# Performance work log

Hardware: AMD Instinct MI355X
Metric: run time of the kernel (lower is better)

Reference implementation:

```python
import jax, jax.numpy as jnp
import numpy as np

N_NODES = 100000
N_EDGES = 1600000
N_GRAPHS = 1024
EMB = 32
HID = 64
N_CLASSES = 10
N_SHAPE = 16
N_COLOR = 8


def setup_inputs() -> dict:
    key = jax.random.key(0)
    ks = jax.random.split(key, 12)
    shape_id = jax.random.randint(ks[0], (N_NODES,), 0, N_SHAPE + 1, dtype=jnp.int32)
    color_id = jax.random.randint(ks[1], (N_NODES,), 0, N_COLOR + 1, dtype=jnp.int32)
    edge_index = jax.random.randint(ks[2], (2, N_EDGES), 0, N_NODES, dtype=jnp.int32)
    batch = jnp.sort(jax.random.randint(ks[3], (N_NODES,), 0, N_GRAPHS, dtype=jnp.int32))
    shape_table = jax.random.normal(ks[4], (N_SHAPE + 1, EMB), jnp.float32)
    color_table = jax.random.normal(ks[5], (N_COLOR + 1, EMB), jnp.float32)
    W1 = jax.random.normal(ks[6], (EMB, HID), jnp.float32) / np.sqrt(EMB)
    b1 = jnp.zeros((HID,), jnp.float32)
    W2 = jax.random.normal(ks[7], (HID, HID), jnp.float32) / np.sqrt(HID)
    b2 = jnp.zeros((HID,), jnp.float32)
    Wl = jax.random.normal(ks[8], (HID, N_CLASSES), jnp.float32) / np.sqrt(HID)
    bl = jnp.zeros((N_CLASSES,), jnp.float32)
    return dict(shape_id=shape_id, color_id=color_id, edge_index=edge_index, batch=batch,
                shape_table=shape_table, color_table=color_table,
                W1=W1, b1=b1, W2=W2, b2=b2, Wl=Wl, bl=bl)


def gcn_conv(x, W, b, src, dst, num_nodes):
    # PyG GCNConv: add self-loops, symmetric normalization D^-1/2 (A+I) D^-1/2
    h = x @ W  # [N, out]
    deg = 1.0 + jax.ops.segment_sum(jnp.ones_like(dst, jnp.float32), dst, num_segments=num_nodes)
    dis = jax.lax.rsqrt(deg)  # deg >= 1 due to self-loop
    norm = dis[src] * dis[dst]  # [E]
    agg = jax.ops.segment_sum(h[src] * norm[:, None], dst, num_segments=num_nodes)
    agg = agg + h * (dis * dis)[:, None]  # self-loop term
    return agg + b


def reference(shape_id, color_id, edge_index, batch, shape_table, color_table,
              W1, b1, W2, b2, Wl, bl):
    # padding_idx=0 -> row 0 contributes zeros
    st = shape_table.at[0].set(0.0)
    ct = color_table.at[0].set(0.0)
    x = st[shape_id] + ct[color_id]  # [N, emb]
    src, dst = edge_index[0], edge_index[1]
    x = jax.nn.relu(gcn_conv(x, W1, b1, src, dst, N_NODES))
    x = jax.nn.relu(gcn_conv(x, W2, b2, src, dst, N_NODES))
    # global_mean_pool over batch ids
    sums = jax.ops.segment_sum(x, batch, num_segments=N_GRAPHS)
    cnts = jax.ops.segment_sum(jnp.ones((x.shape[0],), x.dtype), batch, num_segments=N_GRAPHS)
    pooled = sums / jnp.maximum(cnts, 1.0)[:, None]  # [B, hidden]
    return pooled @ Wl + bl  # [B, num_classes]
```

## Files before the change

### kernel.cpp

```cpp
#include <hip/hip_runtime.h>
#include <hip/hip_bf16.h>
#include <hip/hip_fp16.h>

#define N_NODES   100000
#define N_EDGES   1600000
#define N_GRAPHS  1024
#define EMB       32
#define HID       64
#define N_CLASSES 10
#define SCAN_BLOCKS 391
#define NCOMBO 153
#define BUCK_NODES 448
#define NBUCK 224
#define BIN_CAP 8192
#define EPB 4096
#define PBCAP 11328
#define SENTINEL N_NODES
#define NTILES 6250
#define AGG_GRID 3125

typedef _Float16 f16x8 __attribute__((ext_vector_type(8)));
typedef float f32x4 __attribute__((ext_vector_type(4)));

__global__ __launch_bounds__(256) void prep_kernel(
    const int* __restrict__ sid, const int* __restrict__ cid,
    const int* __restrict__ batch, int* __restrict__ combo, int* __restrict__ gstart,
    const float* __restrict__ st, const float* __restrict__ ct,
    const float* __restrict__ W1, __half* __restrict__ TCh,
    float* __restrict__ pooled, int* __restrict__ gcur, __half* __restrict__ h2s) {
    int t = threadIdx.x;
    int v = blockIdx.x * 256 + t;
    if (v < N_GRAPHS * HID) pooled[v] = 0.0f;
    if (blockIdx.x == 0) {
        if (t < NBUCK) gcur[t] = 0;
        if (t == 0) combo[N_NODES] = 0;
        if (t < 32) ((float*)(h2s + (size_t)N_NODES * HID))[t] = 0.0f;
    }
    if (v < N_NODES) {
        combo[v] = sid[v] * 9 + cid[v];
        int b = batch[v];
        int bp = (v == 0) ? -1 : batch[v - 1];
        for (int g = bp + 1; g <= b; ++g) gstart[g] = v;
        if (v == N_NODES - 1) {
            for (int g = b + 1; g <= N_GRAPHS; ++g) gstart[g] = N_NODES;
        }
    }
    if (blockIdx.x < NCOMBO && t >= 64 && t < 128) {
        int r = blockIdx.x, j = t - 64;
        int s = r / 9, c = r % 9;
        float acc = 0.0f;
        if (s != 0) {
#pragma unroll
            for (int k = 0; k < EMB; ++k) acc = fmaf(st[s * EMB + k], W1[k * HID + j], acc);
        }
        if (c != 0) {
#pragma unroll
            for (int k = 0; k < EMB; ++k) acc = fmaf(ct[c * EMB + k], W1[k * HID + j], acc);
        }
        TCh[r * HID + j] = __float2half_rn(acc);
    }
}

__global__ __launch_bounds__(512) void binA_kernel(
    const int* __restrict__ src, const int* __restrict__ dst,
    int* __restrict__ gcur, int* __restrict__ gbin) {
    __shared__ int2 stg[EPB];
    __shared__ int hist[NBUCK];
    __shared__ int base[NBUCK + 1];
    __shared__ int gstart[NBUCK];
    __shared__ int scanbuf[256];
    int t = threadIdx.x;
    int e0 = blockIdx.x * EPB;
    for (int i = t; i < NBUCK; i += 512) hist[i] = 0;
    __syncthreads();

    int2 myq[8];
    int mybo[8];
    if (e0 + EPB <= N_EDGES) {
        int eb = e0 + t * 8;
        int4 sa4 = *(const int4*)&src[eb];
        int4 sb4 = *(const int4*)&src[eb + 4];
        int4 da4 = *(const int4*)&dst[eb];
        int4 db4 = *(const int4*)&dst[eb + 4];
        int ss[8] = {sa4.x, sa4.y, sa4.z, sa4.w, sb4.x, sb4.y, sb4.z, sb4.w};
        int dd[8] = {da4.x, da4.y, da4.z, da4.w, db4.x, db4.y, db4.z, db4.w};
#pragma unroll
        for (int i = 0; i < 8; ++i) {
            unsigned b = (unsigned)dd[i] / BUCK_NODES;
            int off = atomicAdd(&hist[b], 1);
            myq[i].x = ss[i];
            myq[i].y = dd[i];
            mybo[i] = (int)(b << 16) | off;
        }
    } else {
#pragma unroll
        for (int i = 0; i < 8; ++i) {
            int e = e0 + t * 8 + i;
            if (e < N_EDGES) {
                int d = dst[e];
                unsigned b = (unsigned)d / BUCK_NODES;
                int off = atomicAdd(&hist[b], 1);
                myq[i].x = src[e];
                myq[i].y = d;
                mybo[i] = (int)(b << 16) | off;
            } else {
                mybo[i] = -1;
            }
        }
    }
    __syncthreads();

    int h = (t < NBUCK) ? hist[t] : 0;
    if (t < 256) scanbuf[t] = h;
    __syncthreads();
#pragma unroll
    for (int off = 1; off < 256; off <<= 1) {
        int x = (t < 256 && t >= off) ? scanbuf[t - off] : 0;
        __syncthreads();
        if (t < 256) scanbuf[t] += x;
        __syncthreads();
    }
    if (t < NBUCK) base[t] = scanbuf[t] - h;
    if (t == 0) base[NBUCK] = scanbuf[255];
    __syncthreads();
#pragma unroll
    for (int i = 0; i < 8; ++i) {
        if (mybo[i] >= 0) {
            int b = mybo[i] >> 16, off = mybo[i] & 0xFFFF;
            stg[base[b] + off] = myq[i];
        }
    }
    if (t < NBUCK) {
        int n = hist[t];
        gstart[t] = n ? atomicAdd(&gcur[t], n) : 0;
    }
    __syncthreads();
    int total = base[NBUCK];
    for (int i = t; i < total; i += 512) {
        int2 q = stg[i];
        unsigned b = (unsigned)q.y / BUCK_NODES;
        int local = q.y - (int)b * BUCK_NODES;
        gbin[(size_t)b * BIN_CAP + gstart[b] + (i - base[b])] = q.x | (local << 17);
    }
}

__global__ __launch_bounds__(1024) void bucket_scatter_kernel(
    const int* __restrict__ gbin, const int* __restrict__ gcur,
    float* __restrict__ dis, int* __restrict__ rowptr, int* __restrict__ epack4) {
    __shared__ __align__(16) int pbin[BIN_CAP];
    __shared__ int ldeg[BUCK_NODES];
    __shared__ int rbase[BUCK_NODES];
    __shared__ int s[512];
    int b = blockIdx.x, t = threadIdx.x;
    for (int i = t; i < BUCK_NODES; i += 1024) ldeg[i] = 0;
    __syncthreads();
    int n = gcur[b];
    int nc = (n + 3) >> 2;
    {
        const int4* my4 = (const int4*)(gbin + (size_t)b * BIN_CAP);
        for (int c = t; c < nc; c += 1024) {
            int4 p4 = my4[c];
            ((int4*)pbin)[c] = p4;
            int i0 = c * 4;
            if (i0 + 0 < n) atomicAdd(&ldeg[(unsigned)p4.x >> 17], 1);
            if (i0 + 1 < n) atomicAdd(&ldeg[(unsigned)p4.y >> 17], 1);
            if (i0 + 2 < n) atomicAdd(&ldeg[(unsigned)p4.z >> 17], 1);
            if (i0 + 3 < n) atomicAdd(&ldeg[(unsigned)p4.w >> 17], 1);
        }
    }
    __syncthreads();
    int d = (t < BUCK_NODES) ? ldeg[t] : 0;
    int v = b * BUCK_NODES + t;
    if (t < BUCK_NODES && v < N_NODES) dis[v] = rsqrtf(1.0f + (float)d);
    if (b == 0 && t == 0) dis[N_NODES] = 0.0f;
    int dp = (d + 7) & ~7;
    if (dp > 248) dp = 248;
    if (t < 512) s[t] = dp;
    __syncthreads();
#pragma unroll
    for (int off = 1; off < 512; off <<= 1) {
        int x = (t < 512 && t >= off) ? s[t - off] : 0;
        __syncthreads();
        if (t < 512) s[t] += x;
        __syncthreads();
    }
    int rp = 0;
    if (t < 512) rp = b * PBCAP + s[t] - dp;
    if (t < BUCK_NODES) {
        rbase[t] = rp;
        if (v < N_NODES) rowptr[v] = rp | (dp << 24);
    }
    for (int i = t; i < BUCK_NODES; i += 1024) ldeg[i] = 0;
    __syncthreads();
    if (t < BUCK_NODES) {
        for (int k = d; k < dp; ++k) epack4[rp + k] = SENTINEL;
    }
    for (int i = t; i < n; i += 1024) {
        int p = pbin[i];
        int local = (unsigned)p >> 17;
        int r = atomicAdd(&ldeg[local], 1);
        if (r < 248) epack4[rbase[local] + r] = p & 0x1FFFF;
    }
}

#define AGG_CHUNK(CQ, DQ, LBASE)                                               \
    _Pragma("unroll")                                                          \
    for (int i = 0; i < 8; ++i) {                                              \
        int off = __builtin_amdgcn_readlane((CQ), (LBASE) + i);                \
        int wb  = __builtin_amdgcn_readlane(__float_as_int(DQ), (LBASE) + i);  \
        __half tv = *(const __half*)((const char*)TCs + (off + lane2));        \
        acc = fmaf(__int_as_float(wb), __half2float(tv), acc);                 \
    }

#define AGG_NODE(N, RP, DEG, DV, CO)                                           \
    {                                                                          \
        int deg = (DEG);                                                       \
        int cnt = deg > 32 ? 32 : deg;                                         \
        float acc = 0.0f;                                                      \
        if (cnt > 0)  { AGG_CHUNK(cq1, dq1, (N)*16) }                          \
        if (cnt > 8)  { AGG_CHUNK(cq1, dq1, (N)*16 + 8) }                      \
        if (cnt > 16) { AGG_CHUNK(cq2, dq2, (N)*16) }                          \
        if (cnt > 24) { AGG_CHUNK(cq2, dq2, (N)*16 + 8) }                      \
        if (deg > 32) {                                                        \
            for (int e = (RP) + 32; e < (RP) + deg; ++e) {                     \
                int qx = epack4[e] & 0x1FFFF;                                  \
                float dw = dis[qx];                                            \
                __half tv = *(const __half*)((const char*)TCs +                \
                                             ((combo[qx] << 7) + lane2));      \
                acc = fmaf(dw, __half2float(tv), acc);                         \
            }                                                                  \
        }                                                                      \
        __half hv = *(const __half*)((const char*)TCs + ((CO) + lane2));       \
        float val = (DV) * fmaf(__half2float(hv), (DV), acc) + bias;           \
        val = val > 0.0f ? val : 0.0f;                                         \
        xsA[w * 4 + (N)][lane] = __float2half_rn(val * (DV));                  \
    }

__global__ __launch_bounds__(256, 7) void agg1_mm2_kernel(
    const int* __restrict__ epack4, const int* __restrict__ rowptr,
    const int* __restrict__ combo, const float* __restrict__ dis,
    const __half* __restrict__ TCh, const float* __restrict__ W2,
    const float* __restrict__ b1, __half* __restrict__ h2s) {
    __shared__ __align__(16) __half TCs[NCOMBO * HID];
    __shared__ __align__(16) __half xsA[16][72];
    int t = threadIdx.x;
    int lane = t & 63, w = t >> 6;
    int lane2 = lane * 2;
    int sub = lane >> 4, sl = lane & 15;

    int tile = blockIdx.x;
    int v0 = tile * 16 + w * 4;
    int rb = rowptr[v0 + sub] & 0xFFFFFF;
    int q1x = epack4[rb + sl] & 0x1FFFF;
    int q2x = epack4[rb + 16 + sl] & 0x1FFFF;
    float dq1 = dis[q1x], dq2 = dis[q2x];
    int cq1 = combo[q1x] << 7, cq2 = combo[q2x] << 7;
    int r0p = __builtin_amdgcn_readfirstlane(rowptr[v0]);
    int r1p = __builtin_amdgcn_readfirstlane(rowptr[v0 + 1]);
    int r2p = __builtin_amdgcn_readfirstlane(rowptr[v0 + 2]);
    int r3p = __builtin_amdgcn_readfirstlane(rowptr[v0 + 3]);
    float d0 = dis[v0], d1 = dis[v0 + 1], d2 = dis[v0 + 2], d3 = dis[v0 + 3];
    int o0 = combo[v0] << 7, o1 = combo[v0 + 1] << 7;
    int o2 = combo[v0 + 2] << 7, o3 = combo[v0 + 3] << 7;

    float bias = b1[lane];
    f16x8 bf0, bf1;
    {
        int colw = (w << 4) + (lane & 15);
        int kb = (lane >> 4) * 8;
#pragma unroll
        for (int i = 0; i < 8; ++i) {
            bf0[i] = (_Float16)W2[(kb + i) * HID + colw];
            bf1[i] = (_Float16)W2[(32 + kb + i) * HID + colw];
        }
    }
    {
        const int4* s4 = (const int4*)TCh;
        int4* dd4 = (int4*)TCs;
        for (int i = t; i < NCOMBO * HID * 2 / 16; i += 256) dd4[i] = s4[i];
    }
    __syncthreads();

    for (;;) {
        int ntile = tile + AGG_GRID;
        bool more = ntile < NTILES;
        int nv0 = 0, nq1x = 0, nq2x = 0;
        int nr0p = 0, nr1p = 0, nr2p = 0, nr3p = 0;
        float ndq1 = 0.0f, ndq2 = 0.0f, nd0 = 0.0f, nd1 = 0.0f, nd2 = 0.0f, nd3 = 0.0f;
        int ncq1 = 0, ncq2 = 0, no0 = 0, no1 = 0, no2 = 0, no3 = 0;
        if (more) {
            nv0 = ntile * 16 + w * 4;
            int nrb = rowptr[nv0 + sub] & 0xFFFFFF;
            nq1x = epack4[nrb + sl] & 0x1FFFF;
            nq2x = epack4[nrb + 16 + sl] & 0x1FFFF;
            ndq1 = dis[nq1x]; ndq2 = dis[nq2x];
            ncq1 = combo[nq1x] << 7; ncq2 = combo[nq2x] << 7;
            nr0p = __builtin_amdgcn_readfirstlane(rowptr[nv0]);
            nr1p = __builtin_amdgcn_readfirstlane(rowptr[nv0 + 1]);
            nr2p = __builtin_amdgcn_readfirstlane(rowptr[nv0 + 2]);
            nr3p = __builtin_amdgcn_readfirstlane(rowptr[nv0 + 3]);
            nd0 = dis[nv0]; nd1 = dis[nv0 + 1]; nd2 = dis[nv0 + 2]; nd3 = dis[nv0 + 3];
            no0 = combo[nv0] << 7; no1 = combo[nv0 + 1] << 7;
            no2 = combo[nv0 + 2] << 7; no3 = combo[nv0 + 3] << 7;
        }
        int r0 = r0p & 0xFFFFFF, g0 = (int)((unsigned)r0p >> 24);
        int r1 = r1p & 0xFFFFFF, g1 = (int)((unsigned)r1p >> 24);
        int r2 = r2p & 0xFFFFFF, g2 = (int)((unsigned)r2p >> 24);
        int r3 = r3p & 0xFFFFFF, g3 = (int)((unsigned)r3p >> 24);
        AGG_NODE(0, r0, g0, d0, o0)
        AGG_NODE(1, r1, g1, d1, o1)
        AGG_NODE(2, r2, g2, d2, o2)
        AGG_NODE(3, r3, g3, d3, o3)
        __syncthreads();

        const __half* xa = &xsA[lane & 15][0];
        f16x8 a0 = *(const f16x8*)(xa + (lane >> 4) * 8);
        f16x8 a1 = *(const f16x8*)(xa + 32 + (lane >> 4) * 8);
        __syncthreads();
        f32x4 dacc = {0.0f, 0.0f, 0.0f, 0.0f};
        dacc = __builtin_amdgcn_mfma_f32_16x16x32_f16(a0, bf0, dacc, 0, 0, 0);
        dacc = __builtin_amdgcn_mfma_f32_16x16x32_f16(a1, bf1, dacc, 0, 0, 0);

        __half* Dst = (__half*)xsA;
        {
            int colg = (w << 4) + (lane & 15);
#pragma unroll
            for (int i = 0; i < 4; ++i)
                Dst[((lane >> 4) * 4 + i) * 64 + colg] = __float2half_rn(dacc[i]);
        }
        __syncthreads();

        {
            const uint2* ds2 = (const uint2*)Dst;
            uint2* go = (uint2*)(h2s + (size_t)tile * 16 * HID);
            go[t] = ds2[t];
        }
        if (!more) break;
        __syncthreads();
        tile = ntile; v0 = nv0;
        q1x = nq1x; q2x = nq2x; dq1 = ndq1; dq2 = ndq2; cq1 = ncq1; cq2 = ncq2;
        r0p = nr0p; r1p = nr1p; r2p = nr2p; r3p = nr3p;
        d0 = nd0; d1 = nd1; d2 = nd2; d3 = nd3;
        o0 = no0; o1 = no1; o2 = no2; o3 = no3;
    }
}

__device__ __forceinline__ float agg2_node(const int* __restrict__ epack4, int sx,
                                           int rs, int deg, int lane, int lane2,
                                           const __half* __restrict__ h2s) {
    float acc = 0.0f;
    int p = rs;
    int re = rs + deg;
    for (;;) {
        int avail = re - p;
        int cnt = avail > 64 ? 64 : avail;
        int vo = sx << 7;
        int j = 0;
        for (; j + 16 <= cnt; j += 16) {
            float g[16];
#pragma unroll
            for (int i = 0; i < 16; ++i) {
                int off = __builtin_amdgcn_readlane(vo, j + i);
                g[i] = __half2float(*(const __half*)((const char*)h2s + (off + lane2)));
            }
#pragma unroll
            for (int i = 0; i < 16; ++i) acc += g[i];
        }
        if (j < cnt) {
            float g[8];
#pragma unroll
            for (int i = 0; i < 8; ++i) {
                int off = __builtin_amdgcn_readlane(vo, j + i);
                g[i] = __half2float(*(const __half*)((const char*)h2s + (off + lane2)));
            }
#pragma unroll
            for (int i = 0; i < 8; ++i) acc += g[i];
        }
        p += 64;
        if (p >= re) break;
        sx = epack4[p + lane];
    }
    return acc;
}

__global__ __launch_bounds__(256, 8) void agg2_pool_kernel(
    const int* __restrict__ epack4, const int* __restrict__ rowptr,
    const __half* __restrict__ h2s, const float* __restrict__ dis,
    const float* __restrict__ b2, const int* __restrict__ batch,
    float* __restrict__ pooled) {
    int t = threadIdx.x, lane = t & 63, w = t >> 6;
    int lane2 = lane * 2;
    int v0 = (blockIdx.x * 4 + w) * 4;

    int r0p = __builtin_amdgcn_readfirstlane(rowptr[v0]);
    int r1p = __builtin_amdgcn_readfirstlane(rowptr[v0 + 1]);
    int r2p = __builtin_amdgcn_readfirstlane(rowptr[v0 + 2]);
    int r3p = __builtin_amdgcn_readfirstlane(rowptr[v0 + 3]);
    int r0 = r0p & 0xFFFFFF, dp0 = (int)((unsigned)r0p >> 24);
    int r1 = r1p & 0xFFFFFF, dp1 = (int)((unsigned)r1p >> 24);
    int r2 = r2p & 0xFFFFFF, dp2 = (int)((unsigned)r2p >> 24);
    int r3 = r3p & 0xFFFFFF, dp3 = (int)((unsigned)r3p >> 24);

    int sa = epack4[r0 + lane];
    int sb = epack4[r1 + lane];
    int sc = epack4[r2 + lane];
    int sd = epack4[r3 + lane];

    float bv = b2[lane];
    float acc0 = agg2_node(epack4, sa, r0, dp0, lane, lane2, h2s);
    float acc1 = agg2_node(epack4, sb, r1, dp1, lane, lane2, h2s);
    float acc2 = agg2_node(epack4, sc, r2, dp2, lane, lane2, h2s);
    float acc3 = agg2_node(epack4, sd, r3, dp3, lane, lane2, h2s);

#define AGG2_VAL(V, ACC, OUT)                                                  \
    {                                                                          \
        float dv = dis[V];                                                     \
        float self = __half2float(h2s[(size_t)(V) * HID + lane]);              \
        float val = dv * ((ACC) + self) + bv;                                  \
        OUT = val > 0.0f ? val : 0.0f;                                         \
    }
    float val0, val1, val2, val3;
    AGG2_VAL(v0, acc0, val0)
    AGG2_VAL(v0 + 1, acc1, val1)
    AGG2_VAL(v0 + 2, acc2, val2)
    AGG2_VAL(v0 + 3, acc3, val3)
#undef AGG2_VAL

    int g0 = __builtin_amdgcn_readfirstlane(batch[v0]);
    int g1 = __builtin_amdgcn_readfirstlane(batch[v0 + 1]);
    int g2 = __builtin_amdgcn_readfirstlane(batch[v0 + 2]);
    int g3 = __builtin_amdgcn_readfirstlane(batch[v0 + 3]);
    float s = val0; int g = g0;
    if (g1 == g) { s += val1; } else { unsafeAtomicAdd(&pooled[g * HID + lane], s); g = g1; s = val1; }
    if (g2 == g) { s += val2; } else { unsafeAtomicAdd(&pooled[g * HID + lane], s); g = g2; s = val2; }
    if (g3 == g) { s += val3; } else { unsafeAtomicAdd(&pooled[g * HID + lane], s); g = g3; s = val3; }
    unsafeAtomicAdd(&pooled[g * HID + lane], s);
}

__global__ __launch_bounds__(64) void logits_kernel(
    const float* __restrict__ pooled, const int* __restrict__ gstart,
    const float* __restrict__ Wl, const float* __restrict__ bl,
    float* __restrict__ out) {
    __shared__ float row[HID];
    int g = blockIdx.x, t = threadIdx.x;
    int c = gstart[g + 1] - gstart[g]; if (c < 1) c = 1;
    row[t] = pooled[g * HID + t] / (float)c;
    __syncthreads();
    if (t < N_CLASSES) {
        float acc = bl[t];
#pragma unroll
        for (int k = 0; k < HID; ++k) acc = fmaf(row[k], Wl[k * N_CLASSES + t], acc);
        out[g * N_CLASSES + t] = acc;
    }
}

extern "C" void kernel_launch(void* const* d_in, const int* in_sizes, int n_in,
                              void* d_out, int out_size, void* d_ws, size_t ws_size,
                              hipStream_t stream) {
    const int*   shape_id = (const int*)d_in[0];
    const int*   color_id = (const int*)d_in[1];
    const int*   edge_idx = (const int*)d_in[2];
    const int*   batch    = (const int*)d_in[3];
    const float* st       = (const float*)d_in[4];
    const float* ct       = (const float*)d_in[5];
    const float* W1       = (const float*)d_in[6];
    const float* b1       = (const float*)d_in[7];
    const float* W2       = (const float*)d_in[8];
    const float* b2       = (const float*)d_in[9];
    const float* Wl       = (const float*)d_in[10];
    const float* bl       = (const float*)d_in[11];
    float* out = (float*)d_out;

    const int* src = edge_idx;
    const int* dst = edge_idx + N_EDGES;

    char* ws = (char*)d_ws;
    int*    combo   = (int*)   (ws + 0);
    float*  dis     = (float*) (ws + 400384);
    int*    gstart  = (int*)   (ws + 801792);
    int*    rowptr  = (int*)   (ws + 1201152);
    __half* TCh     = (__half*)(ws + 1603584);
    float*  pooled  = (float*) (ws + 1623552);
    int*    gcur    = (int*)   (ws + 1889792);
    int*    epack4  = (int*)   (ws + 1890816);
    int*    gbin    = (int*)   (ws + 14690816);
    __half* h2s     = (__half*)(ws + 29370880);

    prep_kernel<<<SCAN_BLOCKS, 256, 0, stream>>>(shape_id, color_id, batch, combo, gstart,
                                                 st, ct, W1, TCh, pooled, gcur, h2s);

    binA_kernel<<<(N_EDGES + EPB - 1) / EPB, 512, 0, stream>>>(src, dst, gcur, gbin);

    bucket_scatter_kernel<<<NBUCK, 1024, 0, stream>>>(gbin, gcur, dis, rowptr, epack4);

    agg1_mm2_kernel<<<AGG_GRID, 256, 0, stream>>>(epack4, rowptr, combo, dis, TCh, W2, b1, h2s);

    agg2_pool_kernel<<<6250, 256, 0, stream>>>(epack4, rowptr, h2s, dis, b2, batch, pooled);

    logits_kernel<<<N_GRAPHS, 64, 0, stream>>>(pooled, gstart, Wl, bl, out);
}
```

Measured before the change: 176.4 us.

## Replace barrier-based block scans with wavefront shuffle scans; shrink aggregation grid

The Hillis-Steele shared-memory prefix scans in the binning and bucket-scatter kernels, which needed about two barriers per step, are replaced with intra-wavefront shuffle scans plus a small per-wave sum combine. This cuts the block-wide scan down to a single barrier. Separately, the aggregation kernel's grid size drops from 3125 to 1250 blocks, so each block presumably handles more tiles. The grid change shifts the balance between occupancy and per-block work and may leave some compute units underused.

```diff
diff --git a/kernel.cpp b/kernel.cpp
--- a/kernel.cpp
+++ b/kernel.cpp
@@ -17,7 +17,7 @@
 #define PBCAP 11328
 #define SENTINEL N_NODES
 #define NTILES 6250
-#define AGG_GRID 3125
+#define AGG_GRID 1250
 
 typedef _Float16 f16x8 __attribute__((ext_vector_type(8)));
 typedef float f32x4 __attribute__((ext_vector_type(4)));
@@ -68,7 +68,7 @@
     __shared__ int hist[NBUCK];
     __shared__ int base[NBUCK + 1];
     __shared__ int gstart[NBUCK];
-    __shared__ int scanbuf[256];
+    __shared__ int wsum[4];
     int t = threadIdx.x;
     int e0 = blockIdx.x * EPB;
     for (int i = t; i < NBUCK; i += 512) hist[i] = 0;
@@ -111,17 +111,23 @@
     __syncthreads();
 
     int h = (t < NBUCK) ? hist[t] : 0;
-    if (t < 256) scanbuf[t] = h;
-    __syncthreads();
-#pragma unroll
-    for (int off = 1; off < 256; off <<= 1) {
-        int x = (t < 256 && t >= off) ? scanbuf[t - off] : 0;
-        __syncthreads();
-        if (t < 256) scanbuf[t] += x;
-        __syncthreads();
-    }
-    if (t < NBUCK) base[t] = scanbuf[t] - h;
-    if (t == 0) base[NBUCK] = scanbuf[255];
+    int val = h;
+#pragma unroll
+    for (int off = 1; off < 64; off <<= 1) {
+        int x = __shfl_up(val, off, 64);
+        if ((t & 63) >= off) val += x;
+    }
+    if (t < 256 && (t & 63) == 63) wsum[t >> 6] = val;
+    __syncthreads();
+    if (t < 256) {
+        int wv = t >> 6;
+        int wo = 0;
+#pragma unroll
+        for (int i = 0; i < 4; ++i) if (i < wv) wo += wsum[i];
+        int incl = val + wo;
+        if (t < NBUCK) base[t] = incl - h;
+        if (t == 255) base[NBUCK] = incl;
+    }
     __syncthreads();
 #pragma unroll
     for (int i = 0; i < 8; ++i) {
@@ -150,7 +156,7 @@
     __shared__ __align__(16) int pbin[BIN_CAP];
     __shared__ int ldeg[BUCK_NODES];
     __shared__ int rbase[BUCK_NODES];
-    __shared__ int s[512];
+    __shared__ int wsum[8];
     int b = blockIdx.x, t = threadIdx.x;
     for (int i = t; i < BUCK_NODES; i += 1024) ldeg[i] = 0;
     __syncthreads();
@@ -175,26 +181,31 @@
     if (b == 0 && t == 0) dis[N_NODES] = 0.0f;
     int dp = (d + 7) & ~7;
     if (dp > 248) dp = 248;
-    if (t < 512) s[t] = dp;
-    __syncthreads();
-#pragma unroll
-    for (int off = 1; off < 512; off <<= 1) {
-        int x = (t < 512 && t >= off) ? s[t - off] : 0;
-        __syncthreads();
-        if (t < 512) s[t] += x;
-        __syncthreads();
-    }
-    int rp = 0;
-    if (t < 512) rp = b * PBCAP + s[t] - dp;
-    if (t < BUCK_NODES) {
-        rbase[t] = rp;
-        if (v < N_NODES) rowptr[v] = rp | (dp << 24);
+    int val = (t < 512) ? dp : 0;
+#pragma unroll
+    for (int off = 1; off < 64; off <<= 1) {
+        int x = __shfl_up(val, off, 64);
+        if ((t & 63) >= off) val += x;
+    }
+    if (t < 512 && (t & 63) == 63) wsum[t >> 6] = val;
+    __syncthreads();
+    if (t < 512) {
+        int wv = t >> 6;
+        int wo = 0;
+#pragma unroll
+        for (int i = 0; i < 8; ++i) if (i < wv) wo += wsum[i];
+        int incl = val + wo;
+        int rp = b * PBCAP + incl - dp;
+        if (t < BUCK_NODES) {
+            rbase[t] = rp;
+            if (v < N_NODES) rowptr[v] = rp | (dp << 24);
+        }
+        if (t < BUCK_NODES) {
+            for (int k = d; k < dp; ++k) epack4[rp + k] = SENTINEL;
+        }
     }
     for (int i = t; i < BUCK_NODES; i += 1024) ldeg[i] = 0;
     __syncthreads();
-    if (t < BUCK_NODES) {
-        for (int k = d; k < dp; ++k) epack4[rp + k] = SENTINEL;
-    }
     for (int i = t; i < n; i += 1024) {
         int p = pbin[i];
         int local = (unsigned)p >> 17;
```

Measured after the change: 178.1 us. No clear change (+1.0%).
